# Kernel tuning notes

Measured on AMD Instinct MI355X. Metric: run time of the kernel, lower is better.

Reference implementation:

```python
import jax, jax.numpy as jnp
import numpy as np

EPS_PD = 1e-6      # torch.nn.PairwiseDistance default eps (added to the difference)
EPS_NORM = 1e-12   # F.normalize default eps

B, D, C = 1024, 512, 256  # batch, in_features, out_features


def _l2_normalize(x, axis):
    n = jnp.linalg.norm(x, axis=axis, keepdims=True)
    return x / jnp.maximum(n, EPS_NORM)


def _pairwise_dist(a, b):
    # Faithful to torch PairwiseDistance(p=2) with the unsqueeze(2)/t().unsqueeze(0)
    # broadcast trick: norm over the feature dim of (a[:, :, None] - b.T[None, :, :] + eps).
    # a: [N, D], b: [M, D] -> [N, M]
    diff = a[:, :, None] - b.T[None, :, :] + EPS_PD  # [N, D, M]
    return jnp.sqrt(jnp.sum(diff * diff, axis=1))


def setup_inputs() -> dict:
    key = jax.random.key(0)
    k1, k2, k3 = jax.random.split(key, 3)
    return {
        "features": jax.random.normal(k1, (B, D), dtype=jnp.float32),
        "weights": jax.random.normal(k2, (C, D), dtype=jnp.float32),          # nn.init.normal_(0,1)
        "distance_scale": jax.random.normal(k3, (1,), dtype=jnp.float32),
        "use_distance_scale": 1,
    }


def reference(features, weights, distance_scale, use_distance_scale):
    f = _l2_normalize(features, axis=1)   # [B, D]
    w = _l2_normalize(weights, axis=1)    # [C, D]
    distances = _pairwise_dist(f, w)          # [B, C]
    distances_protoc = _pairwise_dist(w, w)   # [C, C]
    logits = distances - distances_protoc.sum() * 0.1
    if use_distance_scale:
        return -logits * jnp.abs(distance_scale)
    return -logits
```

## Files before the change

kernel.cpp:

```cpp
#include <hip/hip_runtime.h>
#include <math.h>

#define DIMS 512
#define BATCH 1024
#define CLS 256
#define ROWS (BATCH + CLS)

#define EPS_PD 1e-6f
#define DEPS2 (512.0f * 1e-6f * 1e-6f)
#define EPS_NORM 1e-12f


typedef short bf16x8 __attribute__((ext_vector_type(8)));
typedef float f32x4 __attribute__((ext_vector_type(4)));

__device__ __forceinline__ float waveReduceSum(float v) {
#pragma unroll
  for (int off = 32; off > 0; off >>= 1)
    v += __shfl_xor(v, off, 64);
  return v;
}

__device__ __forceinline__ unsigned short f2bf(float x) {
  unsigned int u = __float_as_uint(x);
  u += 0x7fffu + ((u >> 16) & 1u);
  return (unsigned short)(u >> 16);
}

__global__ __launch_bounds__(256) void k_norm(
    const float* __restrict__ feat, const float* __restrict__ wt,
    unsigned short* __restrict__ fnw, float* __restrict__ Srow) {
  const int r = blockIdx.x * 4 + (threadIdx.x >> 6);
  const int lane = threadIdx.x & 63;
  const float* src = (r < BATCH) ? (feat + (size_t)r * DIMS)
                                 : (wt + (size_t)(r - BATCH) * DIMS);
  const float4* s4 = (const float4*)src;

  float4 a = s4[lane * 2];
  float4 c = s4[lane * 2 + 1];

  float ss = a.x*a.x + a.y*a.y + a.z*a.z + a.w*a.w
           + c.x*c.x + c.y*c.y + c.z*c.z + c.w*c.w;
  float sm = a.x + a.y + a.z + a.w + c.x + c.y + c.z + c.w;
  ss = waveReduceSum(ss);
  sm = waveReduceSum(sm);
  const float rn = 1.f / fmaxf(sqrtf(ss), EPS_NORM);

  ushort4 p0, p1;
  p0.x = f2bf(a.x * rn); p0.y = f2bf(a.y * rn);
  p0.z = f2bf(a.z * rn); p0.w = f2bf(a.w * rn);
  p1.x = f2bf(c.x * rn); p1.y = f2bf(c.y * rn);
  p1.z = f2bf(c.z * rn); p1.w = f2bf(c.w * rn);

  unsigned short* dst = fnw + (size_t)(r >> 4) * 8192 + (size_t)lane * 128 + (r & 15) * 8;
  *(ushort4*)dst = p0;
  *(ushort4*)(dst + 4) = p1;

  if (lane == 0) Srow[r] = sm * rn;
}

#define FRAG(g, k0) (*(const bf16x8*)(fnw + (size_t)(g) * 8192 + (k0) * 16 + (size_t)lane * 8))

__global__ __launch_bounds__(256) void k_protoc(
    const unsigned short* __restrict__ fnw, const float* __restrict__ Srow,
    float* __restrict__ partial) {
  const int lane = threadIdx.x & 63;
  const int w = threadIdx.x >> 6;
  const int i0 = blockIdx.y * 64 + (w >> 1) * 32;
  const int j0 = blockIdx.x * 64 + (w & 1) * 32;

  const int gA = (BATCH + i0) >> 4;
  const int gB = (BATCH + j0) >> 4;

  f32x4 acc00 = {0.f,0.f,0.f,0.f}, acc01 = {0.f,0.f,0.f,0.f};
  f32x4 acc10 = {0.f,0.f,0.f,0.f}, acc11 = {0.f,0.f,0.f,0.f};

#pragma unroll
  for (int k0 = 0; k0 < DIMS; k0 += 32) {
    const bf16x8 a0 = FRAG(gA, k0);
    const bf16x8 a1 = FRAG(gA + 1, k0);
    const bf16x8 b0 = FRAG(gB, k0);
    const bf16x8 b1 = FRAG(gB + 1, k0);
    acc00 = __builtin_amdgcn_mfma_f32_16x16x32_bf16(a0, b0, acc00, 0, 0, 0);
    acc01 = __builtin_amdgcn_mfma_f32_16x16x32_bf16(a0, b1, acc01, 0, 0, 0);
    acc10 = __builtin_amdgcn_mfma_f32_16x16x32_bf16(a1, b0, acc10, 0, 0, 0);
    acc11 = __builtin_amdgcn_mfma_f32_16x16x32_bf16(a1, b1, acc11, 0, 0, 0);
  }

  const int crow = ((lane >> 4) & 3) * 4;
  const int ccol = lane & 15;

  const float swj0 = Srow[BATCH + j0 + ccol];
  const float swj1 = Srow[BATCH + j0 + 16 + ccol];

  float s = 0.f;
  const f32x4 accs[4] = {acc00, acc01, acc10, acc11};
#pragma unroll
  for (int hi = 0; hi < 2; ++hi) {
#pragma unroll
    for (int q = 0; q < 4; ++q) {
      const int i = i0 + hi * 16 + crow + q;
      const float swi = Srow[BATCH + i];
#pragma unroll
      for (int hj = 0; hj < 2; ++hj) {
        const int j = j0 + hj * 16 + ccol;
        const float dot = accs[hi * 2 + hj][q];
        const float swj = hj ? swj1 : swj0;
        float dist;
        if (i == j) {
          dist = sqrtf(DEPS2);
        } else {
          const float d2 = 2.f - 2.f * dot + 2.f * EPS_PD * (swi - swj) + DEPS2;
          dist = sqrtf(fmaxf(d2, 0.f));
        }
        s += dist;
      }
    }
  }

  s = waveReduceSum(s);
  if (lane == 0) partial[((blockIdx.y * 4 + blockIdx.x) << 2) + w] = s;
}

__global__ __launch_bounds__(256) void k_main(
    const unsigned short* __restrict__ fnw, const float* __restrict__ Srow,
    const float* __restrict__ partial, const float* __restrict__ dscale,
    const int* __restrict__ use_ds, float* __restrict__ out) {
  const int lane = threadIdx.x & 63;
  const int w = threadIdx.x >> 6;
  const int r0 = blockIdx.x * 64 + (w >> 1) * 32;
  const int j0 = blockIdx.y * 64 + (w & 1) * 32;

  const float myPartial = partial[lane];

  const int gA = r0 >> 4;
  const int gB = (BATCH + j0) >> 4;

  f32x4 acc00 = {0.f,0.f,0.f,0.f}, acc01 = {0.f,0.f,0.f,0.f};
  f32x4 acc10 = {0.f,0.f,0.f,0.f}, acc11 = {0.f,0.f,0.f,0.f};

#pragma unroll
  for (int k0 = 0; k0 < DIMS; k0 += 32) {
    const bf16x8 a0 = FRAG(gA, k0);
    const bf16x8 a1 = FRAG(gA + 1, k0);
    const bf16x8 b0 = FRAG(gB, k0);
    const bf16x8 b1 = FRAG(gB + 1, k0);
    acc00 = __builtin_amdgcn_mfma_f32_16x16x32_bf16(a0, b0, acc00, 0, 0, 0);
    acc01 = __builtin_amdgcn_mfma_f32_16x16x32_bf16(a0, b1, acc01, 0, 0, 0);
    acc10 = __builtin_amdgcn_mfma_f32_16x16x32_bf16(a1, b0, acc10, 0, 0, 0);
    acc11 = __builtin_amdgcn_mfma_f32_16x16x32_bf16(a1, b1, acc11, 0, 0, 0);
  }

  const float S = waveReduceSum(myPartial);
  const float Ssc = 0.1f * S;
  const float sc = (use_ds[0] != 0) ? fabsf(dscale[0]) : 1.0f;

  const int crow = ((lane >> 4) & 3) * 4;
  const int ccol = lane & 15;

  const float swj0 = Srow[BATCH + j0 + ccol];
  const float swj1 = Srow[BATCH + j0 + 16 + ccol];

  const f32x4 accs[4] = {acc00, acc01, acc10, acc11};
#pragma unroll
  for (int hi = 0; hi < 2; ++hi) {
#pragma unroll
    for (int q = 0; q < 4; ++q) {
      const int i = r0 + hi * 16 + crow + q;
      const float sfi = Srow[i];
#pragma unroll
      for (int hj = 0; hj < 2; ++hj) {
        const int j = j0 + hj * 16 + ccol;
        const float dot = accs[hi * 2 + hj][q];
        const float swj = hj ? swj1 : swj0;
        const float d2 = 2.f - 2.f * dot + 2.f * EPS_PD * (sfi - swj) + DEPS2;
        const float dist = sqrtf(fmaxf(d2, 0.f));
        out[(size_t)i * CLS + j] = (Ssc - dist) * sc;
      }
    }
  }
}

extern "C" void kernel_launch(void* const* d_in, const int* in_sizes, int n_in,
                              void* d_out, int out_size, void* d_ws, size_t ws_size,
                              hipStream_t stream) {
  const float* feat = (const float*)d_in[0];
  const float* wt   = (const float*)d_in[1];
  const float* ds   = (const float*)d_in[2];
  const int*   use  = (const int*)d_in[3];
  float* out = (float*)d_out;

  unsigned short* fnw = (unsigned short*)d_ws;
  float* fbase   = (float*)((char*)d_ws + (size_t)ROWS * DIMS * 2);
  float* Srow    = fbase;
  float* partial = fbase + ROWS;

  k_norm<<<ROWS / 4, 256, 0, stream>>>(feat, wt, fnw, Srow);
  k_protoc<<<dim3(4, 4), 256, 0, stream>>>(fnw, Srow, partial);
  k_main<<<dim3(16, 4), 256, 0, stream>>>(fnw, Srow, partial, ds, use, out);
}
```

Measured before the change: 22.45 us.

## Fuse normalize, prototype-sum and main distance kernels with grid barriers

Replaces the three kernel launches with one persistent 80-block kernel. Each wave first normalizes four rows, then all blocks meet at an atomic grid barrier. Next, 64 waves compute the prototype distance partial sums and 256 waves compute the feature-weight dot tiles. A second barrier then lets the main waves write the output. The aim is to remove launch overhead and inter-kernel gaps, at the cost of spin-wait barriers, which assume all 80 blocks are co-resident, and an extra memset launch to reset the counters.

```diff
diff --git a/kernel.cpp b/kernel.cpp
--- a/kernel.cpp
+++ b/kernel.cpp
@@ -5,6 +5,7 @@
 #define BATCH 1024
 #define CLS 256
 #define ROWS (BATCH + CLS)
+#define NBLK 80
 
 #define EPS_PD 1e-6f
 #define DEPS2 (512.0f * 1e-6f * 1e-6f)
@@ -27,49 +28,63 @@
   return (unsigned short)(u >> 16);
 }
 
-__global__ __launch_bounds__(256) void k_norm(
-    const float* __restrict__ feat, const float* __restrict__ wt,
-    unsigned short* __restrict__ fnw, float* __restrict__ Srow) {
-  const int r = blockIdx.x * 4 + (threadIdx.x >> 6);
-  const int lane = threadIdx.x & 63;
-  const float* src = (r < BATCH) ? (feat + (size_t)r * DIMS)
-                                 : (wt + (size_t)(r - BATCH) * DIMS);
-  const float4* s4 = (const float4*)src;
+#define FRAG(g, k0) (*(const bf16x8*)(fnw + (size_t)(g) * 8192 + (k0) * 16 + (size_t)lane * 8))
 
-  float4 a = s4[lane * 2];
-  float4 c = s4[lane * 2 + 1];
-
-  float ss = a.x*a.x + a.y*a.y + a.z*a.z + a.w*a.w
-           + c.x*c.x + c.y*c.y + c.z*c.z + c.w*c.w;
-  float sm = a.x + a.y + a.z + a.w + c.x + c.y + c.z + c.w;
-  ss = waveReduceSum(ss);
-  sm = waveReduceSum(sm);
-  const float rn = 1.f / fmaxf(sqrtf(ss), EPS_NORM);
-
-  ushort4 p0, p1;
-  p0.x = f2bf(a.x * rn); p0.y = f2bf(a.y * rn);
-  p0.z = f2bf(a.z * rn); p0.w = f2bf(a.w * rn);
-  p1.x = f2bf(c.x * rn); p1.y = f2bf(c.y * rn);
-  p1.z = f2bf(c.z * rn); p1.w = f2bf(c.w * rn);
-
-  unsigned short* dst = fnw + (size_t)(r >> 4) * 8192 + (size_t)lane * 128 + (r & 15) * 8;
-  *(ushort4*)dst = p0;
-  *(ushort4*)(dst + 4) = p1;
-
-  if (lane == 0) Srow[r] = sm * rn;
+__device__ __forceinline__ void gridBarrier(unsigned* cnt, unsigned target) {
+  __threadfence();
+  __syncthreads();
+  if (threadIdx.x == 0) {
+    atomicAdd(cnt, 1u);
+    while (atomicAdd(cnt, 0u) < target) {}
+  }
+  __syncthreads();
+  __threadfence();
 }
 
-#define FRAG(g, k0) (*(const bf16x8*)(fnw + (size_t)(g) * 8192 + (k0) * 16 + (size_t)lane * 8))
+__global__ __launch_bounds__(256) void k_fused(
+    const float* __restrict__ feat, const float* __restrict__ wt,
+    const float* __restrict__ dscale, const int* __restrict__ use_ds,
+    unsigned short* __restrict__ fnw, float* __restrict__ Srow,
+    float* __restrict__ partial, unsigned* cnt, float* __restrict__ out) {
+  const int tid = threadIdx.x;
+  const int lane = tid & 63;
+  const int w = tid >> 6;
+  const int W = blockIdx.x * 4 + w;
 
-__global__ __launch_bounds__(256) void k_protoc(
-    const unsigned short* __restrict__ fnw, const float* __restrict__ Srow,
-    float* __restrict__ partial) {
-  const int lane = threadIdx.x & 63;
-  const int w = threadIdx.x >> 6;
-  const int i0 = blockIdx.y * 64 + (w >> 1) * 32;
-  const int j0 = blockIdx.x * 64 + (w & 1) * 32;
+  for (int rr = 0; rr < 4; ++rr) {
+    const int r = W * 4 + rr;
+    const float* src = (r < BATCH) ? (feat + (size_t)r * DIMS)
+                                   : (wt + (size_t)(r - BATCH) * DIMS);
+    const float4* s4 = (const float4*)src;
+    const float4 a = s4[lane * 2];
+    const float4 c = s4[lane * 2 + 1];
 
-  const int gA = (BATCH + i0) >> 4;
+    float ss = a.x*a.x + a.y*a.y + a.z*a.z + a.w*a.w
+             + c.x*c.x + c.y*c.y + c.z*c.z + c.w*c.w;
+    float sm = a.x + a.y + a.z + a.w + c.x + c.y + c.z + c.w;
+    ss = waveReduceSum(ss);
+    sm = waveReduceSum(sm);
+    const float rn = 1.f / fmaxf(sqrtf(ss), EPS_NORM);
+
+    ushort4 p0, p1;
+    p0.x = f2bf(a.x * rn); p0.y = f2bf(a.y * rn);
+    p0.z = f2bf(a.z * rn); p0.w = f2bf(a.w * rn);
+    p1.x = f2bf(c.x * rn); p1.y = f2bf(c.y * rn);
+    p1.z = f2bf(c.z * rn); p1.w = f2bf(c.w * rn);
+
+    unsigned short* dst = fnw + (size_t)(r >> 4) * 8192 + (size_t)lane * 128 + (r & 15) * 8;
+    *(ushort4*)dst = p0;
+    *(ushort4*)(dst + 4) = p1;
+
+    if (lane == 0) Srow[r] = sm * rn;
+  }
+
+  gridBarrier(&cnt[0], NBLK);
+
+  const bool isProtoc = (W < 64);
+  const int iTile = isProtoc ? (W >> 3) * 32 : ((W - 64) >> 3) * 32;
+  const int j0 = (W & 7) * 32;
+  const int gA = (isProtoc ? (BATCH + iTile) : iTile) >> 4;
   const int gB = (BATCH + j0) >> 4;
 
   f32x4 acc00 = {0.f,0.f,0.f,0.f}, acc01 = {0.f,0.f,0.f,0.f};
@@ -89,93 +104,60 @@
 
   const int crow = ((lane >> 4) & 3) * 4;
   const int ccol = lane & 15;
-
   const float swj0 = Srow[BATCH + j0 + ccol];
   const float swj1 = Srow[BATCH + j0 + 16 + ccol];
+  const f32x4 accs[4] = {acc00, acc01, acc10, acc11};
 
-  float s = 0.f;
-  const f32x4 accs[4] = {acc00, acc01, acc10, acc11};
+  if (isProtoc) {
+    float s = 0.f;
 #pragma unroll
-  for (int hi = 0; hi < 2; ++hi) {
+    for (int hi = 0; hi < 2; ++hi) {
 #pragma unroll
-    for (int q = 0; q < 4; ++q) {
-      const int i = i0 + hi * 16 + crow + q;
-      const float swi = Srow[BATCH + i];
+      for (int q = 0; q < 4; ++q) {
+        const int i = iTile + hi * 16 + crow + q;
+        const float swi = Srow[BATCH + i];
 #pragma unroll
-      for (int hj = 0; hj < 2; ++hj) {
-        const int j = j0 + hj * 16 + ccol;
-        const float dot = accs[hi * 2 + hj][q];
-        const float swj = hj ? swj1 : swj0;
-        float dist;
-        if (i == j) {
-          dist = sqrtf(DEPS2);
-        } else {
-          const float d2 = 2.f - 2.f * dot + 2.f * EPS_PD * (swi - swj) + DEPS2;
-          dist = sqrtf(fmaxf(d2, 0.f));
+        for (int hj = 0; hj < 2; ++hj) {
+          const int j = j0 + hj * 16 + ccol;
+          const float dot = accs[hi * 2 + hj][q];
+          const float swj = hj ? swj1 : swj0;
+          float dist;
+          if (i == j) {
+            dist = sqrtf(DEPS2);
+          } else {
+            const float d2 = 2.f - 2.f * dot + 2.f * EPS_PD * (swi - swj) + DEPS2;
+            dist = sqrtf(fmaxf(d2, 0.f));
+          }
+          s += dist;
         }
-        s += dist;
       }
     }
+    s = waveReduceSum(s);
+    if (lane == 0) partial[W] = s;
   }
 
-  s = waveReduceSum(s);
-  if (lane == 0) partial[((blockIdx.y * 4 + blockIdx.x) << 2) + w] = s;
-}
+  gridBarrier(&cnt[1], NBLK);
 
-__global__ __launch_bounds__(256) void k_main(
-    const unsigned short* __restrict__ fnw, const float* __restrict__ Srow,
-    const float* __restrict__ partial, const float* __restrict__ dscale,
-    const int* __restrict__ use_ds, float* __restrict__ out) {
-  const int lane = threadIdx.x & 63;
-  const int w = threadIdx.x >> 6;
-  const int r0 = blockIdx.x * 64 + (w >> 1) * 32;
-  const int j0 = blockIdx.y * 64 + (w & 1) * 32;
-
-  const float myPartial = partial[lane];
-
-  const int gA = r0 >> 4;
-  const int gB = (BATCH + j0) >> 4;
-
-  f32x4 acc00 = {0.f,0.f,0.f,0.f}, acc01 = {0.f,0.f,0.f,0.f};
-  f32x4 acc10 = {0.f,0.f,0.f,0.f}, acc11 = {0.f,0.f,0.f,0.f};
+  if (!isProtoc) {
+    const float S = waveReduceSum(partial[lane]);
+    const float Ssc = 0.1f * S;
+    const float sc = (use_ds[0] != 0) ? fabsf(dscale[0]) : 1.0f;
 
 #pragma unroll
-  for (int k0 = 0; k0 < DIMS; k0 += 32) {
-    const bf16x8 a0 = FRAG(gA, k0);
-    const bf16x8 a1 = FRAG(gA + 1, k0);
-    const bf16x8 b0 = FRAG(gB, k0);
-    const bf16x8 b1 = FRAG(gB + 1, k0);
-    acc00 = __builtin_amdgcn_mfma_f32_16x16x32_bf16(a0, b0, acc00, 0, 0, 0);
-    acc01 = __builtin_amdgcn_mfma_f32_16x16x32_bf16(a0, b1, acc01, 0, 0, 0);
-    acc10 = __builtin_amdgcn_mfma_f32_16x16x32_bf16(a1, b0, acc10, 0, 0, 0);
-    acc11 = __builtin_amdgcn_mfma_f32_16x16x32_bf16(a1, b1, acc11, 0, 0, 0);
-  }
-
-  const float S = waveReduceSum(myPartial);
-  const float Ssc = 0.1f * S;
-  const float sc = (use_ds[0] != 0) ? fabsf(dscale[0]) : 1.0f;
-
-  const int crow = ((lane >> 4) & 3) * 4;
-  const int ccol = lane & 15;
-
-  const float swj0 = Srow[BATCH + j0 + ccol];
-  const float swj1 = Srow[BATCH + j0 + 16 + ccol];
-
-  const f32x4 accs[4] = {acc00, acc01, acc10, acc11};
+    for (int hi = 0; hi < 2; ++hi) {
 #pragma unroll
-  for (int hi = 0; hi < 2; ++hi) {
+      for (int q = 0; q < 4; ++q) {
+        const int i = iTile + hi * 16 + crow + q;
+        const float sfi = Srow[i];
 #pragma unroll
-    for (int q = 0; q < 4; ++q) {
-      const int i = r0 + hi * 16 + crow + q;
-      const float sfi = Srow[i];
-#pragma unroll
-      for (int hj = 0; hj < 2; ++hj) {
-        const int j = j0 + hj * 16 + ccol;
-        const float dot = accs[hi * 2 + hj][q];
-        const float swj = hj ? swj1 : swj0;
-        const float d2 = 2.f - 2.f * dot + 2.f * EPS_PD * (sfi - swj) + DEPS2;
-        const float dist = sqrtf(fmaxf(d2, 0.f));
-        out[(size_t)i * CLS + j] = (Ssc - dist) * sc;
+        for (int hj = 0; hj < 2; ++hj) {
+          const int j = j0 + hj * 16 + ccol;
+          const float dot = accs[hi * 2 + hj][q];
+          const float swj = hj ? swj1 : swj0;
+          const float d2 = 2.f - 2.f * dot + 2.f * EPS_PD * (sfi - swj) + DEPS2;
+          const float dist = sqrtf(fmaxf(d2, 0.f));
+          out[(size_t)i * CLS + j] = (Ssc - dist) * sc;
+        }
       }
     }
   }
@@ -194,8 +176,8 @@
   float* fbase   = (float*)((char*)d_ws + (size_t)ROWS * DIMS * 2);
   float* Srow    = fbase;
   float* partial = fbase + ROWS;
+  unsigned* cnt  = (unsigned*)(partial + 64);
 
-  k_norm<<<ROWS / 4, 256, 0, stream>>>(feat, wt, fnw, Srow);
-  k_protoc<<<dim3(4, 4), 256, 0, stream>>>(fnw, Srow, partial);
-  k_main<<<dim3(16, 4), 256, 0, stream>>>(fnw, Srow, partial, ds, use, out);
+  hipMemsetAsync(cnt, 0, 2 * sizeof(unsigned), stream);
+  k_fused<<<NBLK, 256, 0, stream>>>(feat, wt, ds, use, fnw, Srow, partial, cnt, out);
 }
```

Measured after the change: 46.33 us. +106.4%, slower.
